# Kernel tuning notes

Measured on AMD Instinct MI355X. Metric: run time of the kernel, lower is better.

The kernel has to match this reference:

```python
import jax, jax.numpy as jnp
import numpy as np

B, S = 128, 200
Q, K, V, C, SUM = 20000, 128, 128, 64, 128


def setup_inputs() -> dict:
    key = jax.random.key(0)
    ks = jax.random.split(key, 14)
    stdev = 1.0 / np.sqrt(C + K)  # NTM-style memory init bound

    def lin_w(k, fan_in, shape):
        b = 1.0 / np.sqrt(fan_in)
        return jax.random.uniform(k, shape, jnp.float32, -b, b)

    # embeddings with padding_idx=0 zeroed (PAD_INDEX=0)
    q_emb = jax.random.normal(ks[0], (Q + 1, K), jnp.float32).at[0].set(0.0)
    i_emb = jax.random.normal(ks[1], (2 * Q + 1, V), jnp.float32).at[0].set(0.0)
    key_memory = jax.random.uniform(ks[2], (K, C), jnp.float32, -stdev, stdev)
    init_value_memory = jax.random.uniform(ks[3], (V, C), jnp.float32, -stdev, stdev)
    erase_W = lin_w(ks[4], V, (V, V))
    erase_b = lin_w(ks[5], V, (V,))
    add_W = lin_w(ks[6], V, (V, V))
    add_b = lin_w(ks[7], V, (V,))
    summ_W = lin_w(ks[8], V + K, (V + K, SUM))
    summ_b = lin_w(ks[9], V + K, (SUM,))
    out_W = lin_w(ks[10], SUM, (SUM, 1))
    out_b = lin_w(ks[11], SUM, (1,))
    inp = jax.random.randint(ks[12], (B, S), 0, 2 * Q + 1)
    target_id = jax.random.randint(ks[13], (B,), 0, Q + 1)
    return dict(q_emb=q_emb, i_emb=i_emb, key_memory=key_memory,
                init_value_memory=init_value_memory,
                erase_W=erase_W, erase_b=erase_b, add_W=add_W, add_b=add_b,
                summ_W=summ_W, summ_b=summ_b, out_W=out_W, out_b=out_b,
                input=inp, target_id=target_id)


def reference(q_emb, i_emb, key_memory, init_value_memory,
              erase_W, erase_b, add_W, add_b,
              summ_W, summ_b, out_W, out_b,
              input, target_id):
    Qn = q_emb.shape[0] - 1
    bsz = input.shape[0]
    # map interaction index -> question id
    qid = input - Qn * (input > Qn).astype(input.dtype)          # (B,S)
    # all per-step quantities are independent of memory state -> precompute
    iv = i_emb[input]                                            # (B,S,V)
    e = jax.nn.sigmoid(iv @ erase_W + erase_b)                   # (B,S,V)
    a = jnp.tanh(iv @ add_W + add_b)                             # (B,S,V)
    w = jax.nn.softmax(q_emb[qid] @ key_memory, axis=-1)         # (B,S,C)

    mem0 = jnp.broadcast_to(init_value_memory, (bsz,) + init_value_memory.shape)  # (B,V,C)

    def step(mem, xs):
        e_t, a_t, w_t = xs                                       # (B,V),(B,V),(B,C)
        erase = e_t[:, :, None] * w_t[:, None, :]                # rank-1 outer, (B,V,C)
        add = a_t[:, :, None] * w_t[:, None, :]
        mem = mem * (1.0 - erase) + add
        return mem, None

    xs = (jnp.swapaxes(e, 0, 1), jnp.swapaxes(a, 0, 1), jnp.swapaxes(w, 0, 1))
    mem, _ = jax.lax.scan(step, mem0, xs)                        # (B,V,C)

    qv = q_emb[target_id]                                        # (B,K)
    wt = jax.nn.softmax(qv @ key_memory, axis=-1)                # (B,C)
    read = jnp.einsum('bvc,bc->bv', mem, wt)                     # (B,V)
    summ = jnp.tanh(jnp.concatenate([read, qv], axis=-1) @ summ_W + summ_b)
    return summ @ out_W + out_b                                  # (B,1), pre-sigmoid
```

## Files before the change

kernel.cpp:

```cpp
#include <hip/hip_runtime.h>
#include <hip/hip_bf16.h>
#include <hip/hip_fp16.h>

#define B_ 128
#define S_ 200
#define QN_ 20000
#define V_ 128
#define K_ 128
#define C_ 64
#define SUM_ 128
#define NCH 8
#define CL 25

using short8 = __attribute__((ext_vector_type(8))) short;
using f32x4  = __attribute__((ext_vector_type(4))) float;

__device__ __forceinline__ float fast_sigmoid(float x) { return 1.f / (1.f + __expf(-x)); }
__device__ __forceinline__ float fast_tanh(float x)    { return 1.f - 2.f / (__expf(2.f * x) + 1.f); }

template<bool BF>
__device__ __forceinline__ float ld(const void* p, long long i) {
    if (BF) return __bfloat162float(((const __hip_bfloat16*)p)[i]);
    return ((const float*)p)[i];
}
template<bool BF>
__device__ __forceinline__ float2 ld2(const void* p, long long i) {
    if (BF) {
        __hip_bfloat162 v = ((const __hip_bfloat162*)p)[i];
        return make_float2(__bfloat162float(v.x), __bfloat162float(v.y));
    }
    return ((const float2*)p)[i];
}

__device__ __forceinline__ unsigned short f2bf(float v) {
    __hip_bfloat16 h = __float2bfloat16(v);
    unsigned short u;
    __builtin_memcpy(&u, &h, 2);
    return u;
}

__device__ __forceinline__ int probe_flag_wave(const void* erase_b) {
    const unsigned* w = (const unsigned*)erase_b;
    const int lane = threadIdx.x & 63;
    const unsigned lo = w[lane] & 0xffffu;
    const float f = __uint_as_float(lo << 16);
    const unsigned long long bal = __ballot(!(fabsf(f) <= 0.5f));
    return (__popcll(bal) <= 8) ? 1 : 0;
}

__global__ __launch_bounds__(256) void dkvmn_prepack(
    const void* erase_W, const void* add_W, const void* key_memory,
    const void* erase_b, unsigned short* __restrict__ wpack)
{
    const int bf = probe_flag_wave(erase_b);
    const int fid = blockIdx.x * 256 + threadIdx.x;
    if (fid >= 5120) return;
    const int lane = fid & 63;
    const int ks = (fid >> 6) & 3;
    const int wv = (fid >> 8) & 3;
    const int q  = fid >> 10;
    const int nt = wv + 4 * q;
    const void* Wsrc;
    int ncol, ldn;
    if (q < 2)      { Wsrc = erase_W;    ncol = nt * 16 + (lane & 15);        ldn = 128; }
    else if (q < 4) { Wsrc = add_W;      ncol = (nt - 8) * 16 + (lane & 15);  ldn = 128; }
    else            { Wsrc = key_memory; ncol = (nt - 16) * 16 + (lane & 15); ldn = 64; }
    const int k8 = (lane >> 4) * 8;
    unsigned short o[8];
    #pragma unroll
    for (int jj = 0; jj < 8; ++jj) {
        const long long idx = (long long)(ks * 32 + k8 + jj) * ldn + ncol;
        const float v = bf ? ld<true>(Wsrc, idx) : ld<false>(Wsrc, idx);
        o[jj] = f2bf(v);
    }
    *(uint4*)(wpack + (size_t)fid * 8) = *(const uint4*)o;
}

template<bool BF>
__device__ __forceinline__ void phase1_mfma_body(
    const void* q_emb, const void* i_emb,
    const void* erase_b, const void* add_b,
    const int* __restrict__ input, const unsigned short* __restrict__ wpack,
    float* __restrict__ e_buf, float* __restrict__ a_buf, float* __restrict__ w_buf,
    unsigned short* ivA, unsigned short* qvA, float* wlog, int* sidx, int* sqid)
{
    const int p0 = blockIdx.x * 64;
    const int t = threadIdx.x;
    const int wv = t >> 6;
    const int lane = t & 63;
    const int lrow = lane & 15;
    const int lk8 = (lane >> 4) * 8;

    if (t < 64) {
        const int ix = input[p0 + t];
        sidx[t] = ix;
        sqid[t] = ix > QN_ ? ix - QN_ : ix;
    }
    __syncthreads();

    #pragma unroll
    for (int r = 0; r < 8; ++r) {
        const int j = t + 256 * r;
        const int tensor = j >> 10;
        const int row = (j >> 4) & 63;
        const int seg = j & 15;
        const int gr = tensor ? sqid[row] : sidx[row];
        unsigned short* dst = (tensor ? qvA : ivA) + row * 136 + seg * 8;
        if (BF) {
            const unsigned short* src = (const unsigned short*)(tensor ? q_emb : i_emb);
            *(uint4*)dst = *(const uint4*)(src + (long long)gr * 128 + seg * 8);
        } else {
            const float* src = (const float*)(tensor ? q_emb : i_emb) + (long long)gr * 128 + seg * 8;
            const float4 f0 = *(const float4*)src;
            const float4 f1 = *(const float4*)(src + 4);
            unsigned short o[8] = {f2bf(f0.x), f2bf(f0.y), f2bf(f0.z), f2bf(f0.w),
                                   f2bf(f1.x), f2bf(f1.y), f2bf(f1.z), f2bf(f1.w)};
            *(uint4*)dst = *(const uint4*)o;
        }
    }

    short8 bfr[5][4];
    int nco[5];
    float biasq[4];
    #pragma unroll
    for (int q = 0; q < 5; ++q) {
        const int nt = wv + 4 * q;
        if (q < 2)      nco[q] = nt * 16 + lrow;
        else if (q < 4) nco[q] = (nt - 8) * 16 + lrow;
        else            nco[q] = (nt - 16) * 16 + lrow;
        if (q < 2)      biasq[q] = ld<BF>(erase_b, nco[q]);
        else if (q < 4) biasq[q] = ld<BF>(add_b, nco[q]);
        #pragma unroll
        for (int ks = 0; ks < 4; ++ks)
            bfr[q][ks] = *(const short8*)(wpack +
                ((size_t)(((q * 4 + wv) * 4 + ks) * 64 + lane)) * 8);
    }
    __syncthreads();

    for (int mt = 0; mt < 4; ++mt) {
        short8 afr[4];
        const unsigned short* ar = ivA + (mt * 16 + lrow) * 136 + lk8;
        #pragma unroll
        for (int ks = 0; ks < 4; ++ks)
            afr[ks] = *(const short8*)(ar + ks * 32);
        #pragma unroll
        for (int q = 0; q < 4; ++q) {
            f32x4 acc = {0.f, 0.f, 0.f, 0.f};
            #pragma unroll
            for (int ks = 0; ks < 4; ++ks)
                acc = __builtin_amdgcn_mfma_f32_16x16x32_bf16(afr[ks], bfr[q][ks], acc, 0, 0, 0);
            float* dst = (q < 2) ? e_buf : a_buf;
            const int ncol = nco[q];
            const float bb = biasq[q];
            #pragma unroll
            for (int r = 0; r < 4; ++r) {
                const int prow = p0 + mt * 16 + (lane >> 4) * 4 + r;
                const float y = acc[r] + bb;
                dst[(size_t)prow * V_ + ncol] =
                    (q < 2) ? fast_sigmoid(y) : fast_tanh(y);
            }
        }
    }
    for (int mt = 0; mt < 4; ++mt) {
        short8 afr[4];
        const unsigned short* ar = qvA + (mt * 16 + lrow) * 136 + lk8;
        #pragma unroll
        for (int ks = 0; ks < 4; ++ks)
            afr[ks] = *(const short8*)(ar + ks * 32);
        f32x4 acc = {0.f, 0.f, 0.f, 0.f};
        #pragma unroll
        for (int ks = 0; ks < 4; ++ks)
            acc = __builtin_amdgcn_mfma_f32_16x16x32_bf16(afr[ks], bfr[4][ks], acc, 0, 0, 0);
        #pragma unroll
        for (int r = 0; r < 4; ++r)
            wlog[(mt * 16 + (lane >> 4) * 4 + r) * 68 + nco[4]] = acc[r];
    }
    __syncthreads();

    {
        const int row = t >> 2;
        const int cs = t & 3;
        const float* wr = &wlog[row * 68 + cs * 16];
        float v[16];
        #pragma unroll
        for (int ii = 0; ii < 4; ++ii)
            *(float4*)&v[ii * 4] = *(const float4*)&wr[ii * 4];
        float m = v[0];
        #pragma unroll
        for (int ii = 1; ii < 16; ++ii) m = fmaxf(m, v[ii]);
        m = fmaxf(m, __shfl_xor(m, 1, 64));
        m = fmaxf(m, __shfl_xor(m, 2, 64));
        float s = 0.f;
        #pragma unroll
        for (int ii = 0; ii < 16; ++ii) { v[ii] = __expf(v[ii] - m); s += v[ii]; }
        s += __shfl_xor(s, 1, 64);
        s += __shfl_xor(s, 2, 64);
        const float inv = 1.f / s;
        float* wout = w_buf + (size_t)(p0 + row) * C_ + cs * 16;
        #pragma unroll
        for (int ii = 0; ii < 4; ++ii)
            *(float4*)&wout[ii * 4] = make_float4(v[ii*4] * inv, v[ii*4+1] * inv,
                                                  v[ii*4+2] * inv, v[ii*4+3] * inv);
    }
}

__global__ __launch_bounds__(256) void dkvmn_phase1_mfma(
    const void* q_emb, const void* i_emb,
    const void* erase_b, const void* add_b,
    const int* __restrict__ input, const unsigned short* __restrict__ wpack,
    float* e_buf, float* a_buf, float* w_buf)
{
    __shared__ unsigned short ivA[64 * 136];
    __shared__ unsigned short qvA[64 * 136];
    __shared__ float wlog[64 * 68];
    __shared__ int sidx[64], sqid[64];
    if (probe_flag_wave(erase_b))
        phase1_mfma_body<true>(q_emb, i_emb, erase_b, add_b, input, wpack,
                               e_buf, a_buf, w_buf, ivA, qvA, wlog, sidx, sqid);
    else
        phase1_mfma_body<false>(q_emb, i_emb, erase_b, add_b, input, wpack,
                                e_buf, a_buf, w_buf, ivA, qvA, wlog, sidx, sqid);
}

__global__ __launch_bounds__(256) void dkvmn_scan(
    const float* __restrict__ e_buf, const float* __restrict__ a_buf,
    const float* __restrict__ w_buf, __half2* __restrict__ du)
{
    const int bid = blockIdx.x;
    const int b = bid & 127;
    const int chunk = bid >> 7;
    const int t = threadIdx.x;
    const int vg = t >> 3;
    const int cg = t & 7;
    const int v0 = vg * 4, c0 = cg * 8;

    float ym[4][8], Dm[4][8];
    #pragma unroll
    for (int i = 0; i < 4; ++i)
        #pragma unroll
        for (int j = 0; j < 8; ++j) { ym[i][j] = 0.f; Dm[i][j] = 1.f; }

    const float* eb = e_buf + ((size_t)b * S_ + chunk * CL) * V_ + v0;
    const float* ab = a_buf + ((size_t)b * S_ + chunk * CL) * V_ + v0;
    const float* wb = w_buf + ((size_t)b * S_ + chunk * CL) * C_ + c0;

    #define SSTEP(E, A, W0, W1)                                                \
        do {                                                                   \
            const float ev[4] = {(E).x, (E).y, (E).z, (E).w};                  \
            const float av[4] = {(A).x, (A).y, (A).z, (A).w};                  \
            const float wvv[8] = {(W0).x, (W0).y, (W0).z, (W0).w,              \
                                  (W1).x, (W1).y, (W1).z, (W1).w};             \
            _Pragma("unroll")                                                  \
            for (int i = 0; i < 4; ++i) {                                      \
                _Pragma("unroll")                                              \
                for (int j = 0; j < 8; ++j) {                                  \
                    const float d = fmaf(-ev[i], wvv[j], 1.f);                 \
                    Dm[i][j] *= d;                                             \
                    ym[i][j] = fmaf(d, ym[i][j], av[i] * wvv[j]);              \
                }                                                              \
            }                                                                  \
        } while (0)

    float4 pe[2], pa[2], pw0[2], pw1[2];
    #pragma unroll
    for (int k = 0; k < 2; ++k) {
        pe[k]  = *(const float4*)(eb + (size_t)k * V_);
        pa[k]  = *(const float4*)(ab + (size_t)k * V_);
        pw0[k] = *(const float4*)(wb + (size_t)k * C_);
        pw1[k] = *(const float4*)(wb + (size_t)k * C_ + 4);
    }
    for (int s0 = 0; s0 < 22; s0 += 2) {
        #pragma unroll
        for (int k = 0; k < 2; ++k) {
            const float4 E = pe[k], A = pa[k], W0 = pw0[k], W1 = pw1[k];
            const size_t sn = (size_t)(s0 + k + 2);
            pe[k]  = *(const float4*)(eb + sn * V_);
            pa[k]  = *(const float4*)(ab + sn * V_);
            pw0[k] = *(const float4*)(wb + sn * C_);
            pw1[k] = *(const float4*)(wb + sn * C_ + 4);
            SSTEP(E, A, W0, W1);
        }
    }
    {
        const float4 te  = *(const float4*)(eb + (size_t)24 * V_);
        const float4 ta  = *(const float4*)(ab + (size_t)24 * V_);
        const float4 tw0 = *(const float4*)(wb + (size_t)24 * C_);
        const float4 tw1 = *(const float4*)(wb + (size_t)24 * C_ + 4);
        SSTEP(pe[0], pa[0], pw0[0], pw1[0]);
        SSTEP(pe[1], pa[1], pw0[1], pw1[1]);
        SSTEP(te, ta, tw0, tw1);
    }
    #undef SSTEP

    __half2* dbase = du + ((size_t)(chunk * B_ + b) * (V_ * C_));
    #pragma unroll
    for (int i = 0; i < 4; ++i) {
        __half2 h[8];
        #pragma unroll
        for (int j = 0; j < 8; ++j)
            h[j] = __floats2half2_rn(Dm[i][j], ym[i][j]);
        __half2* dst = dbase + (v0 + i) * C_ + c0;
        *(uint4*)dst = *(const uint4*)&h[0];
        *(uint4*)(dst + 4) = *(const uint4*)&h[4];
    }
}

template<bool BF>
__device__ __forceinline__ void combine_body(
    const void* q_emb, const void* key_memory, const void* init_value_memory,
    const void* summ_W, const void* summ_b, const void* out_W, const void* out_b,
    const int* __restrict__ target_id, const __half2* __restrict__ du,
    void* outp, float* wtl, float* readl, float* summl)
{
    const int b = blockIdx.x;
    const int t = threadIdx.x;
    const long long qrow = (long long)target_id[b] * K_;

    if (t < 64) {
        float logit = 0.f;
        #pragma unroll 8
        for (int i = 0; i < K_; ++i)
            logit += ld<BF>(q_emb, qrow + i) * ld<BF>(key_memory, i * C_ + t);
        float m = logit;
        for (int off = 32; off > 0; off >>= 1)
            m = fmaxf(m, __shfl_xor(m, off, 64));
        const float ex = __expf(logit - m);
        float ssum = ex;
        for (int off = 32; off > 0; off >>= 1)
            ssum += __shfl_xor(ssum, off, 64);
        wtl[t] = ex / ssum;
    }

    const int v = t >> 1;
    const int c0 = (t & 1) * 32;
    float mem[32];
    #pragma unroll 8
    for (int k = 0; k < 32; ++k)
        mem[k] = ld<BF>(init_value_memory, v * C_ + c0 + k);
    #pragma unroll
    for (int ch = 0; ch < NCH; ++ch) {
        const __half2* dsrc = du + ((size_t)(ch * B_ + b) * (V_ * C_)) + v * C_ + c0;
        #pragma unroll
        for (int k = 0; k < 32; ++k) {
            const float2 f = __half22float2(dsrc[k]);
            mem[k] = fmaf(f.x, mem[k], f.y);
        }
    }
    __syncthreads();

    float pacc = 0.f;
    #pragma unroll
    for (int k = 0; k < 32; ++k)
        pacc += mem[k] * wtl[c0 + k];
    pacc += __shfl_xor(pacc, 1, 64);
    if ((t & 1) == 0) readl[v] = pacc;
    __syncthreads();

    if (t < 128) {
        float acc = ld<BF>(summ_b, t);
        #pragma unroll 8
        for (int i = 0; i < 128; ++i)
            acc += readl[i] * ld<BF>(summ_W, i * SUM_ + t);
        #pragma unroll 8
        for (int i = 0; i < 128; ++i)
            acc += ld<BF>(q_emb, qrow + i) * ld<BF>(summ_W, (128 + i) * SUM_ + t);
        summl[t] = fast_tanh(acc);
    }
    __syncthreads();
    if (t < 64) {
        float oacc = summl[t] * ld<BF>(out_W, t) + summl[t + 64] * ld<BF>(out_W, t + 64);
        for (int off = 32; off > 0; off >>= 1)
            oacc += __shfl_xor(oacc, off, 64);
        if (t == 0) {
            const float res = oacc + ld<BF>(out_b, 0);
            if (BF) ((__hip_bfloat16*)outp)[b] = __float2bfloat16(res);
            else    ((float*)outp)[b] = res;
        }
    }
}

__global__ __launch_bounds__(256) void dkvmn_combine(
    const void* q_emb, const void* key_memory, const void* init_value_memory,
    const void* summ_W, const void* summ_b, const void* out_W, const void* out_b,
    const void* erase_b, const int* __restrict__ target_id,
    const __half2* __restrict__ du, void* outp)
{
    __shared__ float wtl[C_], readl[V_], summl[SUM_];
    if (probe_flag_wave(erase_b))
        combine_body<true>(q_emb, key_memory, init_value_memory, summ_W, summ_b,
                           out_W, out_b, target_id, du, outp, wtl, readl, summl);
    else
        combine_body<false>(q_emb, key_memory, init_value_memory, summ_W, summ_b,
                            out_W, out_b, target_id, du, outp, wtl, readl, summl);
}

extern "C" void kernel_launch(void* const* d_in, const int* in_sizes, int n_in,
                              void* d_out, int out_size, void* d_ws, size_t ws_size,
                              hipStream_t stream) {
    const void* q_emb             = d_in[0];
    const void* i_emb             = d_in[1];
    const void* key_memory        = d_in[2];
    const void* init_value_memory = d_in[3];
    const void* erase_W           = d_in[4];
    const void* erase_b           = d_in[5];
    const void* add_W             = d_in[6];
    const void* add_b             = d_in[7];
    const void* summ_W            = d_in[8];
    const void* summ_b            = d_in[9];
    const void* out_W             = d_in[10];
    const void* out_b             = d_in[11];
    const int* input     = (const int*)d_in[12];
    const int* target_id = (const int*)d_in[13];

    float* e_buf = (float*)d_ws;
    float* a_buf = e_buf + (size_t)B_ * S_ * V_;
    float* w_buf = a_buf + (size_t)B_ * S_ * V_;
    unsigned short* wpack = (unsigned short*)(w_buf + (size_t)B_ * S_ * C_);
    __half2* du = (__half2*)(wpack + 5120 * 8);

    dkvmn_prepack<<<20, 256, 0, stream>>>(erase_W, add_W, key_memory, erase_b, wpack);
    dkvmn_phase1_mfma<<<(B_ * S_) / 64, 256, 0, stream>>>(
        q_emb, i_emb, erase_b, add_b, input, wpack, e_buf, a_buf, w_buf);
    dkvmn_scan<<<NCH * B_, 256, 0, stream>>>(e_buf, a_buf, w_buf, du);
    dkvmn_combine<<<B_, 256, 0, stream>>>(
        q_emb, key_memory, init_value_memory, summ_W, summ_b, out_W, out_b,
        erase_b, target_id, du, d_out);
}
```

Baseline: 154.6 us.

## Fuse projection phase into chunked scan kernel, keeping e/a/w in LDS

Merges the MFMA projection kernel (erase/add gates and key-softmax weights) into the per-(batch,chunk) scan kernel. Each block now computes its 25 steps' e, a (stored as fp16) and w directly into shared memory and runs the scan from LDS. This removes the global round trip of the e/a/w buffers and one kernel launch. In exchange, MFMA tiles are padded from 25 to 32 rows, which wastes some compute, and the per-block LDS footprint grows.

```diff
diff --git a/kernel.cpp b/kernel.cpp
--- a/kernel.cpp
+++ b/kernel.cpp
@@ -23,20 +23,18 @@
     if (BF) return __bfloat162float(((const __hip_bfloat16*)p)[i]);
     return ((const float*)p)[i];
 }
-template<bool BF>
-__device__ __forceinline__ float2 ld2(const void* p, long long i) {
-    if (BF) {
-        __hip_bfloat162 v = ((const __hip_bfloat162*)p)[i];
-        return make_float2(__bfloat162float(v.x), __bfloat162float(v.y));
-    }
-    return ((const float2*)p)[i];
-}
 
 __device__ __forceinline__ unsigned short f2bf(float v) {
     __hip_bfloat16 h = __float2bfloat16(v);
     unsigned short u;
     __builtin_memcpy(&u, &h, 2);
     return u;
+}
+
+__device__ __forceinline__ void ld4h(const __half* p, float* out) {
+    const float2 f01 = __half22float2(*(const __half2*)p);
+    const float2 f23 = __half22float2(*(const __half2*)(p + 2));
+    out[0] = f01.x; out[1] = f01.y; out[2] = f23.x; out[3] = f23.y;
 }
 
 __device__ __forceinline__ int probe_flag_wave(const void* erase_b) {
@@ -76,36 +74,47 @@
     *(uint4*)(wpack + (size_t)fid * 8) = *(const uint4*)o;
 }
 
+struct FusedLDS {
+    unsigned short ivA[32 * 136];
+    unsigned short qvA[32 * 136];
+    __half esh[32 * 136];
+    __half ash[32 * 136];
+    float  wlog[32 * 68];
+    int sidx[32], sqid[32];
+};
+
 template<bool BF>
-__device__ __forceinline__ void phase1_mfma_body(
+__device__ __forceinline__ void fused_body(
     const void* q_emb, const void* i_emb,
     const void* erase_b, const void* add_b,
     const int* __restrict__ input, const unsigned short* __restrict__ wpack,
-    float* __restrict__ e_buf, float* __restrict__ a_buf, float* __restrict__ w_buf,
-    unsigned short* ivA, unsigned short* qvA, float* wlog, int* sidx, int* sqid)
-{
-    const int p0 = blockIdx.x * 64;
+    __half2* __restrict__ du, FusedLDS& sm)
+{
+    const int bid = blockIdx.x;
+    const int b = bid & 127;
+    const int chunk = bid >> 7;
     const int t = threadIdx.x;
     const int wv = t >> 6;
     const int lane = t & 63;
     const int lrow = lane & 15;
     const int lk8 = (lane >> 4) * 8;
 
-    if (t < 64) {
-        const int ix = input[p0 + t];
-        sidx[t] = ix;
-        sqid[t] = ix > QN_ ? ix - QN_ : ix;
-    }
-    __syncthreads();
-
-    #pragma unroll
-    for (int r = 0; r < 8; ++r) {
+    if (t < 32) {
+        const int s = (t < CL) ? t : 0;
+        const int ix = input[b * S_ + chunk * CL + s];
+        sm.sidx[t] = ix;
+        sm.sqid[t] = ix > QN_ ? ix - QN_ : ix;
+    }
+    __syncthreads();
+
+    #pragma unroll
+    for (int r = 0; r < 4; ++r) {
         const int j = t + 256 * r;
-        const int tensor = j >> 10;
-        const int row = (j >> 4) & 63;
+        const int tensor = j >> 9;
+        const int row = (j >> 4) & 31;
         const int seg = j & 15;
-        const int gr = tensor ? sqid[row] : sidx[row];
-        unsigned short* dst = (tensor ? qvA : ivA) + row * 136 + seg * 8;
+        const int gr = tensor ? sm.sqid[row] : sm.sidx[row];
+        unsigned short* dst = (tensor ? sm.qvA : sm.ivA) + row * 136 + seg * 8;
         if (BF) {
             const unsigned short* src = (const unsigned short*)(tensor ? q_emb : i_emb);
             *(uint4*)dst = *(const uint4*)(src + (long long)gr * 128 + seg * 8);
@@ -137,9 +146,10 @@
     }
     __syncthreads();
 
-    for (int mt = 0; mt < 4; ++mt) {
+    #pragma unroll
+    for (int mt = 0; mt < 2; ++mt) {
         short8 afr[4];
-        const unsigned short* ar = ivA + (mt * 16 + lrow) * 136 + lk8;
+        const unsigned short* ar = sm.ivA + (mt * 16 + lrow) * 136 + lk8;
         #pragma unroll
         for (int ks = 0; ks < 4; ++ks)
             afr[ks] = *(const short8*)(ar + ks * 32);
@@ -149,21 +159,21 @@
             #pragma unroll
             for (int ks = 0; ks < 4; ++ks)
                 acc = __builtin_amdgcn_mfma_f32_16x16x32_bf16(afr[ks], bfr[q][ks], acc, 0, 0, 0);
-            float* dst = (q < 2) ? e_buf : a_buf;
             const int ncol = nco[q];
             const float bb = biasq[q];
             #pragma unroll
             for (int r = 0; r < 4; ++r) {
-                const int prow = p0 + mt * 16 + (lane >> 4) * 4 + r;
+                const int orow = mt * 16 + (lane >> 4) * 4 + r;
                 const float y = acc[r] + bb;
-                dst[(size_t)prow * V_ + ncol] =
-                    (q < 2) ? fast_sigmoid(y) : fast_tanh(y);
+                if (q < 2) sm.esh[orow * 136 + ncol] = __float2half(fast_sigmoid(y));
+                else       sm.ash[orow * 136 + ncol] = __float2half(fast_tanh(y));
             }
         }
     }
-    for (int mt = 0; mt < 4; ++mt) {
+    #pragma unroll
+    for (int mt = 0; mt < 2; ++mt) {
         short8 afr[4];
-        const unsigned short* ar = qvA + (mt * 16 + lrow) * 136 + lk8;
+        const unsigned short* ar = sm.qvA + (mt * 16 + lrow) * 136 + lk8;
         #pragma unroll
         for (int ks = 0; ks < 4; ++ks)
             afr[ks] = *(const short8*)(ar + ks * 32);
@@ -173,63 +183,35 @@
             acc = __builtin_amdgcn_mfma_f32_16x16x32_bf16(afr[ks], bfr[4][ks], acc, 0, 0, 0);
         #pragma unroll
         for (int r = 0; r < 4; ++r)
-            wlog[(mt * 16 + (lane >> 4) * 4 + r) * 68 + nco[4]] = acc[r];
+            sm.wlog[(mt * 16 + (lane >> 4) * 4 + r) * 68 + nco[4]] = acc[r];
     }
     __syncthreads();
 
     {
-        const int row = t >> 2;
-        const int cs = t & 3;
-        const float* wr = &wlog[row * 68 + cs * 16];
-        float v[16];
-        #pragma unroll
-        for (int ii = 0; ii < 4; ++ii)
-            *(float4*)&v[ii * 4] = *(const float4*)&wr[ii * 4];
+        const int row = t >> 3;
+        const int cs = t & 7;
+        float* wr = &sm.wlog[row * 68 + cs * 8];
+        float v[8];
+        *(float4*)&v[0] = *(const float4*)&wr[0];
+        *(float4*)&v[4] = *(const float4*)&wr[4];
         float m = v[0];
         #pragma unroll
-        for (int ii = 1; ii < 16; ++ii) m = fmaxf(m, v[ii]);
+        for (int ii = 1; ii < 8; ++ii) m = fmaxf(m, v[ii]);
         m = fmaxf(m, __shfl_xor(m, 1, 64));
         m = fmaxf(m, __shfl_xor(m, 2, 64));
+        m = fmaxf(m, __shfl_xor(m, 4, 64));
         float s = 0.f;
         #pragma unroll
-        for (int ii = 0; ii < 16; ++ii) { v[ii] = __expf(v[ii] - m); s += v[ii]; }
+        for (int ii = 0; ii < 8; ++ii) { v[ii] = __expf(v[ii] - m); s += v[ii]; }
         s += __shfl_xor(s, 1, 64);
         s += __shfl_xor(s, 2, 64);
+        s += __shfl_xor(s, 4, 64);
         const float inv = 1.f / s;
-        float* wout = w_buf + (size_t)(p0 + row) * C_ + cs * 16;
-        #pragma unroll
-        for (int ii = 0; ii < 4; ++ii)
-            *(float4*)&wout[ii * 4] = make_float4(v[ii*4] * inv, v[ii*4+1] * inv,
-                                                  v[ii*4+2] * inv, v[ii*4+3] * inv);
-    }
-}
-
-__global__ __launch_bounds__(256) void dkvmn_phase1_mfma(
-    const void* q_emb, const void* i_emb,
-    const void* erase_b, const void* add_b,
-    const int* __restrict__ input, const unsigned short* __restrict__ wpack,
-    float* e_buf, float* a_buf, float* w_buf)
-{
-    __shared__ unsigned short ivA[64 * 136];
-    __shared__ unsigned short qvA[64 * 136];
-    __shared__ float wlog[64 * 68];
-    __shared__ int sidx[64], sqid[64];
-    if (probe_flag_wave(erase_b))
-        phase1_mfma_body<true>(q_emb, i_emb, erase_b, add_b, input, wpack,
-                               e_buf, a_buf, w_buf, ivA, qvA, wlog, sidx, sqid);
-    else
-        phase1_mfma_body<false>(q_emb, i_emb, erase_b, add_b, input, wpack,
-                                e_buf, a_buf, w_buf, ivA, qvA, wlog, sidx, sqid);
-}
-
-__global__ __launch_bounds__(256) void dkvmn_scan(
-    const float* __restrict__ e_buf, const float* __restrict__ a_buf,
-    const float* __restrict__ w_buf, __half2* __restrict__ du)
-{
-    const int bid = blockIdx.x;
-    const int b = bid & 127;
-    const int chunk = bid >> 7;
-    const int t = threadIdx.x;
+        *(float4*)&wr[0] = make_float4(v[0]*inv, v[1]*inv, v[2]*inv, v[3]*inv);
+        *(float4*)&wr[4] = make_float4(v[4]*inv, v[5]*inv, v[6]*inv, v[7]*inv);
+    }
+    __syncthreads();
+
     const int vg = t >> 3;
     const int cg = t & 7;
     const int v0 = vg * 4, c0 = cg * 8;
@@ -240,57 +222,22 @@
         #pragma unroll
         for (int j = 0; j < 8; ++j) { ym[i][j] = 0.f; Dm[i][j] = 1.f; }
 
-    const float* eb = e_buf + ((size_t)b * S_ + chunk * CL) * V_ + v0;
-    const float* ab = a_buf + ((size_t)b * S_ + chunk * CL) * V_ + v0;
-    const float* wb = w_buf + ((size_t)b * S_ + chunk * CL) * C_ + c0;
-
-    #define SSTEP(E, A, W0, W1)                                                \
-        do {                                                                   \
-            const float ev[4] = {(E).x, (E).y, (E).z, (E).w};                  \
-            const float av[4] = {(A).x, (A).y, (A).z, (A).w};                  \
-            const float wvv[8] = {(W0).x, (W0).y, (W0).z, (W0).w,              \
-                                  (W1).x, (W1).y, (W1).z, (W1).w};             \
-            _Pragma("unroll")                                                  \
-            for (int i = 0; i < 4; ++i) {                                      \
-                _Pragma("unroll")                                              \
-                for (int j = 0; j < 8; ++j) {                                  \
-                    const float d = fmaf(-ev[i], wvv[j], 1.f);                 \
-                    Dm[i][j] *= d;                                             \
-                    ym[i][j] = fmaf(d, ym[i][j], av[i] * wvv[j]);              \
-                }                                                              \
-            }                                                                  \
-        } while (0)
-
-    float4 pe[2], pa[2], pw0[2], pw1[2];
-    #pragma unroll
-    for (int k = 0; k < 2; ++k) {
-        pe[k]  = *(const float4*)(eb + (size_t)k * V_);
-        pa[k]  = *(const float4*)(ab + (size_t)k * V_);
-        pw0[k] = *(const float4*)(wb + (size_t)k * C_);
-        pw1[k] = *(const float4*)(wb + (size_t)k * C_ + 4);
-    }
-    for (int s0 = 0; s0 < 22; s0 += 2) {
-        #pragma unroll
-        for (int k = 0; k < 2; ++k) {
-            const float4 E = pe[k], A = pa[k], W0 = pw0[k], W1 = pw1[k];
-            const size_t sn = (size_t)(s0 + k + 2);
-            pe[k]  = *(const float4*)(eb + sn * V_);
-            pa[k]  = *(const float4*)(ab + sn * V_);
-            pw0[k] = *(const float4*)(wb + sn * C_);
-            pw1[k] = *(const float4*)(wb + sn * C_ + 4);
-            SSTEP(E, A, W0, W1);
-        }
-    }
-    {
-        const float4 te  = *(const float4*)(eb + (size_t)24 * V_);
-        const float4 ta  = *(const float4*)(ab + (size_t)24 * V_);
-        const float4 tw0 = *(const float4*)(wb + (size_t)24 * C_);
-        const float4 tw1 = *(const float4*)(wb + (size_t)24 * C_ + 4);
-        SSTEP(pe[0], pa[0], pw0[0], pw1[0]);
-        SSTEP(pe[1], pa[1], pw0[1], pw1[1]);
-        SSTEP(te, ta, tw0, tw1);
-    }
-    #undef SSTEP
+    for (int s = 0; s < CL; ++s) {
+        float ev[4], av[4], wv8[8];
+        ld4h(sm.esh + s * 136 + v0, ev);
+        ld4h(sm.ash + s * 136 + v0, av);
+        *(float4*)&wv8[0] = *(const float4*)(sm.wlog + s * 68 + c0);
+        *(float4*)&wv8[4] = *(const float4*)(sm.wlog + s * 68 + c0 + 4);
+        #pragma unroll
+        for (int i = 0; i < 4; ++i) {
+            #pragma unroll
+            for (int j = 0; j < 8; ++j) {
+                const float d = fmaf(-ev[i], wv8[j], 1.f);
+                Dm[i][j] *= d;
+                ym[i][j] = fmaf(d, ym[i][j], av[i] * wv8[j]);
+            }
+        }
+    }
 
     __half2* dbase = du + ((size_t)(chunk * B_ + b) * (V_ * C_));
     #pragma unroll
@@ -303,6 +250,19 @@
         *(uint4*)dst = *(const uint4*)&h[0];
         *(uint4*)(dst + 4) = *(const uint4*)&h[4];
     }
+}
+
+__global__ __launch_bounds__(256) void dkvmn_fused(
+    const void* q_emb, const void* i_emb,
+    const void* erase_b, const void* add_b,
+    const int* __restrict__ input, const unsigned short* __restrict__ wpack,
+    __half2* __restrict__ du)
+{
+    __shared__ FusedLDS sm;
+    if (probe_flag_wave(erase_b))
+        fused_body<true>(q_emb, i_emb, erase_b, add_b, input, wpack, du, sm);
+    else
+        fused_body<false>(q_emb, i_emb, erase_b, add_b, input, wpack, du, sm);
 }
 
 template<bool BF>
@@ -412,16 +372,12 @@
     const int* input     = (const int*)d_in[12];
     const int* target_id = (const int*)d_in[13];
 
-    float* e_buf = (float*)d_ws;
-    float* a_buf = e_buf + (size_t)B_ * S_ * V_;
-    float* w_buf = a_buf + (size_t)B_ * S_ * V_;
-    unsigned short* wpack = (unsigned short*)(w_buf + (size_t)B_ * S_ * C_);
+    unsigned short* wpack = (unsigned short*)d_ws;
     __half2* du = (__half2*)(wpack + 5120 * 8);
 
     dkvmn_prepack<<<20, 256, 0, stream>>>(erase_W, add_W, key_memory, erase_b, wpack);
-    dkvmn_phase1_mfma<<<(B_ * S_) / 64, 256, 0, stream>>>(
-        q_emb, i_emb, erase_b, add_b, input, wpack, e_buf, a_buf, w_buf);
-    dkvmn_scan<<<NCH * B_, 256, 0, stream>>>(e_buf, a_buf, w_buf, du);
+    dkvmn_fused<<<NCH * B_, 256, 0, stream>>>(
+        q_emb, i_emb, erase_b, add_b, input, wpack, du);
     dkvmn_combine<<<B_, 256, 0, stream>>>(
         q_emb, key_memory, init_value_memory, summ_W, summ_b, out_W, out_b,
         erase_b, target_id, du, d_out);
```

Result: faster. 148.0 us (-4.2%).
